# Optimization experiments

Hardware: AMD Instinct MI355X
Metric: run time of the kernel (lower is better)

The kernel has to match this reference:

```python
import jax, jax.numpy as jnp
import numpy as np

B, T, TC = 128, 300, 20          # batch, words per sentence, chars per word
DW, DC = 16, 32                  # word / char embedding dims
UC, UM = 32, 64                  # char-LSTM units, main-LSTM units
POS, PAR = 20, 8                 # extra feature dims
VW, VC = 1834, 132               # vocab sizes
DIN = DW + UC + POS + PAR        # 76, input dim of main BiLSTM


def setup_inputs() -> dict:
    key = jax.random.key(0)
    ks = jax.random.split(key, 16)
    s = 0.05
    f32 = jnp.float32
    return dict(
        word_in=jax.random.randint(ks[0], (B, T), 0, VW, dtype=jnp.int32),
        char_in=jax.random.randint(ks[1], (B, T, TC), 0, VC, dtype=jnp.int32),
        input_pos=jax.random.normal(ks[2], (B, T, POS), f32),
        input_par=jax.random.normal(ks[3], (B, T, PAR), f32),
        emb_wor=jax.random.normal(ks[4], (VW, DW), f32) * s,
        emb_char=jax.random.normal(ks[5], (VC, DC), f32) * s,
        char_Wx=jax.random.normal(ks[6], (DC, 4 * UC), f32) * s,
        char_Wh=jax.random.normal(ks[7], (UC, 4 * UC), f32) * s,
        char_b=jnp.zeros((4 * UC,), f32),
        fwd_Wx=jax.random.normal(ks[8], (DIN, 4 * UM), f32) * s,
        fwd_Wh=jax.random.normal(ks[9], (UM, 4 * UM), f32) * s,
        fwd_b=jnp.zeros((4 * UM,), f32),
        bwd_Wx=jax.random.normal(ks[10], (DIN, 4 * UM), f32) * s,
        bwd_Wh=jax.random.normal(ks[11], (UM, 4 * UM), f32) * s,
        bwd_b=jnp.zeros((4 * UM,), f32),
        dense_W=jax.random.normal(ks[12], (2 * UM, 4), f32) * s,
        dense_b=jnp.zeros((4,), f32),
    )


def _lstm(x, mask, Wx, Wh, b):
    """Masked Keras-style LSTM (gate order i,f,g,o). x:(N,S,D) mask:(N,S) bool.
    Masked steps carry state (Keras mask_zero semantics). Returns (N,S,U)."""
    U = Wh.shape[0]
    xz = jnp.einsum('nsd,df->nsf', x, Wx) + b  # hoist input projection out of scan

    def step(carry, inp):
        h, c = carry
        z_x, m = inp
        z = z_x + h @ Wh
        i, f, g, o = jnp.split(z, 4, axis=-1)
        c_new = jax.nn.sigmoid(f) * c + jax.nn.sigmoid(i) * jnp.tanh(g)
        h_new = jax.nn.sigmoid(o) * jnp.tanh(c_new)
        m = m[:, None]
        h = jnp.where(m, h_new, h)
        c = jnp.where(m, c_new, c)
        return (h, c), h

    N = x.shape[0]
    h0 = jnp.zeros((N, U), x.dtype)
    (_, _), hs = jax.lax.scan(step, (h0, h0),
                              (jnp.swapaxes(xz, 0, 1), jnp.swapaxes(mask, 0, 1)))
    return jnp.swapaxes(hs, 0, 1)


def reference(word_in, char_in, input_pos, input_par,
              emb_wor, emb_char, char_Wx, char_Wh, char_b,
              fwd_Wx, fwd_Wh, fwd_b, bwd_Wx, bwd_Wh, bwd_b,
              dense_W, dense_b):
    # word embeddings: (B,T,DW)
    ew = emb_wor[word_in]
    # char embeddings, TimeDistributed over words: (B*T, TC, DC)
    ec = emb_char[char_in].reshape(B * T, TC, DC)
    cmask = (char_in != 0).reshape(B * T, TC)
    # char LSTM, return_sequences=False -> final (last-valid) state
    ch = _lstm(ec, cmask, char_Wx, char_Wh, char_b)[:, -1, :].reshape(B, T, UC)
    # concat word emb, char encoding, extra features -> (B,T,DIN)
    x = jnp.concatenate([ew, ch, input_pos, input_par], axis=-1)
    wmask = word_in != 0
    hf = _lstm(x, wmask, fwd_Wx, fwd_Wh, fwd_b)
    hb = _lstm(x[:, ::-1], wmask[:, ::-1], bwd_Wx, bwd_Wh, bwd_b)[:, ::-1]
    h = jnp.concatenate([hf, hb], axis=-1)  # (B,T,2*UM)
    return jax.nn.softmax(h @ dense_W + dense_b, axis=-1)  # (B,T,4)
```

## Files before the change

### kernel.cpp

```cpp
#include <hip/hip_runtime.h>
#include <hip/hip_bf16.h>

#define B_ 128
#define T_ 300
#define TC_ 20
#define DW_ 16
#define DC_ 32
#define UC_ 32
#define UM_ 64
#define POS_ 20
#define PAR_ 8
#define VW_ 1834
#define VC_ 132
#define DIN_ 76
#define XS_ 80
#define NROW (B_*T_)

typedef _Float16 half_t;
typedef half_t h2 __attribute__((ext_vector_type(2)));

__device__ __forceinline__ float fast_sig(float x){
  return __builtin_amdgcn_rcpf(1.f + __expf(-x));
}
__device__ __forceinline__ float fast_tanh(float x){
  return __builtin_amdgcn_rcpf(1.f + __expf(-2.f*x))*2.f - 1.f;
}
__device__ __forceinline__ float dot2u(unsigned int a, unsigned int b, float acc){
  union{unsigned int u; h2 h;} x, y; x.u = a; y.u = b;
#if __has_builtin(__builtin_amdgcn_fdot2)
  return __builtin_amdgcn_fdot2(x.h, y.h, acc, false);
#else
  return acc + (float)x.h.x*(float)y.h.x + (float)x.h.y*(float)y.h.y;
#endif
}
__device__ __forceinline__ h2 u2h(unsigned int x){
  union{unsigned int u; h2 h;} t; t.u = x; return t.h;
}
__device__ __forceinline__ float us2f(unsigned short s){
  union{unsigned short s; half_t h;} x; x.s = s; return (float)x.h;
}
__device__ __forceinline__ unsigned int packh2(float a, float b){
  union{h2 h; unsigned int u;} cv; cv.h = h2{(half_t)a,(half_t)b}; return cv.u;
}

__global__ void k_prep(const float* __restrict__ emb_char, const float* __restrict__ char_Wx,
                       const float* __restrict__ char_b,  const float* __restrict__ char_Wh,
                       const float* __restrict__ Whf, const float* __restrict__ Whb,
                       const float* __restrict__ Wxf, const float* __restrict__ Wxb,
                       float* __restrict__ xzc, half_t* __restrict__ chT,
                       half_t* __restrict__ whT_h, half_t* __restrict__ wxT_h){
  int id = blockIdx.x*256 + threadIdx.x;
  if (id < 16896){
    int v = id >> 7, j = id & 127;
    float acc = char_b[j];
    #pragma unroll
    for (int k=0;k<DC_;k++) acc += emb_char[v*DC_+k]*char_Wx[k*(4*UC_)+j];
    xzc[id] = acc;
  } else if (id < 20992){
    int t = id - 16896;
    int j = t >> 5, k = t & 31;
    chT[t] = (half_t)char_Wh[k*(4*UC_)+j];
  } else if (id < 53760){
    int t = id - 20992;
    int dirr = t >> 14, j = (t >> 6) & 255, k = t & 63;
    const float* W = dirr ? Whb : Whf;
    whT_h[t] = (half_t)W[k*(4*UM_)+j];
  } else {
    int t = id - 53760;
    int dirr = t / 24576;
    int r = t % 24576;
    int jj = r / 96, k = r % 96;
    const float* W = dirr ? Wxb : Wxf;
    wxT_h[t] = (k < DIN_) ? (half_t)W[k*(4*UM_)+jj] : (half_t)0.f;
  }
}

__global__ __launch_bounds__(512,2) void k_char(const int* __restrict__ char_in,
        const float* __restrict__ xzc, const half_t* __restrict__ chT,
        const int* __restrict__ word_in, const float* __restrict__ emb_wor,
        const float* __restrict__ pos, const float* __restrict__ par,
        float* __restrict__ x){
  __shared__ unsigned int hbuf2[8][16];
  __shared__ float2 zex[8][64];
  __shared__ int sidx[8*TC_];
  const int tid = threadIdx.x;
  const int w8 = tid >> 6;
  const int lane = tid & 63;
  const int u = lane & 31;
  const int half = lane >> 5;
  const int seq = blockIdx.x*8 + w8;

  if (tid < 384){
    int r8 = tid / 48, c48 = tid % 48;
    int row = blockIdx.x*8 + r8;
    int col = (c48 < 16) ? c48 : (c48 + 32);
    float v;
    if (col < DW_)              v = emb_wor[word_in[row]*DW_ + col];
    else if (col < DW_+UC_+POS_) v = pos[row*POS_ + (col-(DW_+UC_))];
    else                         v = par[row*PAR_ + (col-(DW_+UC_+POS_))];
    x[row*XS_ + col] = v;
  }

  if (tid < 8*TC_) sidx[tid] = char_in[blockIdx.x*(8*TC_) + tid];
  if (half==0 && u<16) hbuf2[w8][u] = 0;

  unsigned int wa[16], wb[16];
  {
    const uint4* pa = reinterpret_cast<const uint4*>(chT + (half*64+u)*32);
    const uint4* pb = reinterpret_cast<const uint4*>(chT + (half*64+32+u)*32);
    #pragma unroll
    for (int q=0;q<4;q++){
      uint4 va = pa[q], vb = pb[q];
      wa[q*4+0]=va.x; wa[q*4+1]=va.y; wa[q*4+2]=va.z; wa[q*4+3]=va.w;
      wb[q*4+0]=vb.x; wb[q*4+1]=vb.y; wb[q*4+2]=vb.z; wb[q*4+3]=vb.w;
    }
  }
  __syncthreads();

  float h = 0.f, c = 0.f;
  int idx = sidx[w8*TC_ + 0];
  float za0 = xzc[idx*(4*UC_) + half*64 + u];
  float zb0 = xzc[idx*(4*UC_) + half*64 + 32 + u];

  for (int t=0; t<TC_; t++){
    int idxn = (t+1 < TC_) ? sidx[w8*TC_ + t+1] : 0;
    float zan = xzc[idxn*(4*UC_) + half*64 + u];
    float zbn = xzc[idxn*(4*UC_) + half*64 + 32 + u];

    float za = za0, zb = zb0;
    const uint4* hb = reinterpret_cast<const uint4*>(&hbuf2[w8][0]);
    uint4 q0=hb[0], q1=hb[1], q2=hb[2], q3=hb[3];
    unsigned int hu[16] = {q0.x,q0.y,q0.z,q0.w, q1.x,q1.y,q1.z,q1.w,
                           q2.x,q2.y,q2.z,q2.w, q3.x,q3.y,q3.z,q3.w};
    #pragma unroll
    for (int k=0;k<16;k++){
      za = dot2u(wa[k], hu[k], za);
      zb = dot2u(wb[k], hu[k], zb);
    }
    zex[w8][lane] = make_float2(za, zb);
    if (half == 0){
      float2 p = zex[w8][32+u];
      float zi = za, zf = zb, zg = p.x, zo = p.y;
      float cn = fast_sig(zf)*c + fast_sig(zi)*fast_tanh(zg);
      float hn = fast_sig(zo)*fast_tanh(cn);
      bool m = (idx != 0);
      c = m ? cn : c;
      h = m ? hn : h;
      reinterpret_cast<half_t*>(&hbuf2[w8][0])[u] = (half_t)h;
    }
    idx = idxn; za0 = zan; zb0 = zbn;
  }
  if (half == 0) x[seq*XS_ + DW_ + u] = h;
}

__global__ __launch_bounds__(512,2) void k_xz(const float* __restrict__ x,
      const half_t* __restrict__ wxT_h,
      const float* __restrict__ b_f, const float* __restrict__ b_b,
      half_t* __restrict__ xz){
  __shared__ unsigned int xs[16][40];
  const int j = threadIdx.x;
  const int jj = j & 255;
  const bool bwd = (j >= 256);
  const float bj = bwd ? b_b[jj] : b_f[jj];
  const int u = jj & 63, g = jj >> 6;
  const int ocol = (bwd ? 256 : 0) + u*4 + g;

  unsigned int wq[40];
  {
    const uint4* p = reinterpret_cast<const uint4*>(wxT_h + (size_t)((bwd?256:0)+jj)*96);
    #pragma unroll
    for (int q=0;q<10;q++){
      uint4 v = p[q];
      wq[q*4+0]=v.x; wq[q*4+1]=v.y; wq[q*4+2]=v.z; wq[q*4+3]=v.w;
    }
  }

  const int rowbase = blockIdx.x*16;
  for (int i=j; i<16*40; i+=512){
    int r = i/40, q = i%40;
    unsigned int pk = 0;
    if (q < 38){
      float v0 = x[(size_t)(rowbase+r)*XS_ + 2*q];
      float v1 = x[(size_t)(rowbase+r)*XS_ + 2*q+1];
      pk = packh2(v0, v1);
    }
    xs[r][q] = pk;
  }
  __syncthreads();

  for (int r=0; r<16; r++){
    const uint4* xr = reinterpret_cast<const uint4*>(&xs[r][0]);
    float acc = bj;
    #pragma unroll
    for (int q=0;q<10;q++){
      uint4 v = xr[q];
      acc = dot2u(wq[q*4+0], v.x, acc);
      acc = dot2u(wq[q*4+1], v.y, acc);
      acc = dot2u(wq[q*4+2], v.z, acc);
      acc = dot2u(wq[q*4+3], v.w, acc);
    }
    xz[(size_t)(rowbase+r)*512 + ocol] = (half_t)acc;
  }
}

__global__ __launch_bounds__(64,1) void k_rnn(const half_t* __restrict__ xz,
      const int* __restrict__ word_in, const half_t* __restrict__ whT_h,
      half_t* __restrict__ hcat){
  __shared__ half_t hbuf[64];
  __shared__ int wm[T_];
  const int l = threadIdx.x;
  const int dir = blockIdx.x & 1;
  const int b = blockIdx.x >> 1;

  unsigned int wt[4][32];
  #pragma unroll
  for (int g=0; g<4; g++){
    const uint4* p = reinterpret_cast<const uint4*>(whT_h + ((size_t)dir*256 + g*64 + l)*64);
    #pragma unroll
    for (int q=0;q<8;q++){
      uint4 v = p[q];
      wt[g][q*4+0]=v.x; wt[g][q*4+1]=v.y; wt[g][q*4+2]=v.z; wt[g][q*4+3]=v.w;
    }
  }
  for (int t=l; t<T_; t+=64) wm[t] = word_in[b*T_ + (dir ? (T_-1-t) : t)];
  hbuf[l] = (half_t)0.f;
  __syncthreads();

  float h = 0.f, c_ = 0.f;
  int row0 = b*T_ + (dir ? T_-1 : 0);
  const half_t* xp = xz + (size_t)row0*512 + dir*256 + l*4;
  const ptrdiff_t dstep = dir ? -512 : 512;
  half_t* hout = hcat + (size_t)row0*(2*UM_) + dir*UM_ + l;
  const ptrdiff_t hstep = dir ? -(2*UM_) : (2*UM_);

  ushort4 z0 = *reinterpret_cast<const ushort4*>(xp);
  ushort4 z1 = *reinterpret_cast<const ushort4*>(xp + dstep);
  half_t hh[10];
  const h2 zero2 = {(half_t)0.f, (half_t)0.f};

  for (int outer=0; outer<30; ++outer){
    #pragma unroll
    for (int s=0; s<10; ++s){
      const int t = outer*10 + s;
      ushort4 z2 = {0,0,0,0};
      if (t+2 < T_) z2 = *reinterpret_cast<const ushort4*>(xp + 2*dstep);

      const uint4* hb = reinterpret_cast<const uint4*>(hbuf);
      h2 aI0=zero2, aI1=zero2, aF0=zero2, aF1=zero2;
      h2 aG0=zero2, aG1=zero2, aO0=zero2, aO1=zero2;
      #pragma unroll
      for (int q=0;q<8;q++){
        uint4 hv = hb[q];
        h2 h0=u2h(hv.x), h1=u2h(hv.y), hx=u2h(hv.z), h3=u2h(hv.w);
        aI0 = u2h(wt[0][q*4+0])*h0 + aI0; aI1 = u2h(wt[0][q*4+1])*h1 + aI1;
        aI0 = u2h(wt[0][q*4+2])*hx + aI0; aI1 = u2h(wt[0][q*4+3])*h3 + aI1;
        aF0 = u2h(wt[1][q*4+0])*h0 + aF0; aF1 = u2h(wt[1][q*4+1])*h1 + aF1;
        aF0 = u2h(wt[1][q*4+2])*hx + aF0; aF1 = u2h(wt[1][q*4+3])*h3 + aF1;
        aG0 = u2h(wt[2][q*4+0])*h0 + aG0; aG1 = u2h(wt[2][q*4+1])*h1 + aG1;
        aG0 = u2h(wt[2][q*4+2])*hx + aG0; aG1 = u2h(wt[2][q*4+3])*h3 + aG1;
        aO0 = u2h(wt[3][q*4+0])*h0 + aO0; aO1 = u2h(wt[3][q*4+1])*h1 + aO1;
        aO0 = u2h(wt[3][q*4+2])*hx + aO0; aO1 = u2h(wt[3][q*4+3])*h3 + aO1;
      }
      float zi = us2f(z0.x) + (((float)aI0.x + (float)aI0.y) + ((float)aI1.x + (float)aI1.y));
      float zf = us2f(z0.y) + (((float)aF0.x + (float)aF0.y) + ((float)aF1.x + (float)aF1.y));
      float zg = us2f(z0.z) + (((float)aG0.x + (float)aG0.y) + ((float)aG1.x + (float)aG1.y));
      float zo = us2f(z0.w) + (((float)aO0.x + (float)aO0.y) + ((float)aO1.x + (float)aO1.y));

      int mw = wm[t];
      float cn = fast_sig(zf)*c_ + fast_sig(zi)*fast_tanh(zg);
      float hn = fast_sig(zo)*fast_tanh(cn);
      if (mw != 0){ c_ = cn; h = hn; }
      half_t hq = (half_t)h;
      hbuf[l] = hq;
      hh[s] = hq;
      z0 = z1; z1 = z2; xp += dstep;
    }
    #pragma unroll
    for (int s=0; s<10; ++s) hout[(ptrdiff_t)s * hstep] = hh[s];
    hout += (ptrdiff_t)10 * hstep;
  }
}

__global__ void k_dense(const half_t* __restrict__ hcat, const float* __restrict__ W,
                        const float* __restrict__ bias, float* __restrict__ out){
  int r = blockIdx.x*256 + threadIdx.x;
  const uint4* h4 = reinterpret_cast<const uint4*>(hcat + (size_t)r*(2*UM_));
  float a0=bias[0], a1=bias[1], a2=bias[2], a3=bias[3];
  #pragma unroll
  for (int k8=0;k8<16;k8++){
    uint4 v = h4[k8];
    unsigned int uu[4] = {v.x, v.y, v.z, v.w};
    #pragma unroll
    for (int e=0;e<4;e++){
      int k = k8*8 + e*2;
      float hA = us2f((unsigned short)(uu[e] & 0xffffu));
      float hB = us2f((unsigned short)(uu[e] >> 16));
      a0 += hA*W[k*4+0] + hB*W[(k+1)*4+0];
      a1 += hA*W[k*4+1] + hB*W[(k+1)*4+1];
      a2 += hA*W[k*4+2] + hB*W[(k+1)*4+2];
      a3 += hA*W[k*4+3] + hB*W[(k+1)*4+3];
    }
  }
  float mx = fmaxf(fmaxf(a0,a1), fmaxf(a2,a3));
  float e0=__expf(a0-mx), e1=__expf(a1-mx), e2=__expf(a2-mx), e3=__expf(a3-mx);
  float s = __builtin_amdgcn_rcpf(e0+e1+e2+e3);
  out[r*4+0]=e0*s; out[r*4+1]=e1*s; out[r*4+2]=e2*s; out[r*4+3]=e3*s;
}

extern "C" void kernel_launch(void* const* d_in, const int* in_sizes, int n_in,
                              void* d_out, int out_size, void* d_ws, size_t ws_size,
                              hipStream_t stream) {
  const int*   word_in  = (const int*)  d_in[0];
  const int*   char_in  = (const int*)  d_in[1];
  const float* inp_pos  = (const float*)d_in[2];
  const float* inp_par  = (const float*)d_in[3];
  const float* emb_wor  = (const float*)d_in[4];
  const float* emb_char = (const float*)d_in[5];
  const float* char_Wx  = (const float*)d_in[6];
  const float* char_Wh  = (const float*)d_in[7];
  const float* char_b   = (const float*)d_in[8];
  const float* fwd_Wx   = (const float*)d_in[9];
  const float* fwd_Wh   = (const float*)d_in[10];
  const float* fwd_b    = (const float*)d_in[11];
  const float* bwd_Wx   = (const float*)d_in[12];
  const float* bwd_Wh   = (const float*)d_in[13];
  const float* bwd_b    = (const float*)d_in[14];
  const float* dense_W  = (const float*)d_in[15];
  const float* dense_b  = (const float*)d_in[16];
  float* out = (float*)d_out;

  char* base = (char*)d_ws;
  float*  xw    = (float*)base;            base += (size_t)NROW*XS_*4;
  half_t* hcat  = (half_t*)base;           base += (size_t)NROW*128*2;
  float*  xzc   = (float*)base;            base += (size_t)VC_*128*4;
  half_t* chT   = (half_t*)base;           base += 128*32*2;
  half_t* whT_h = (half_t*)base;           base += 2*256*64*2;
  half_t* wxT_h = (half_t*)base;           base += 2*256*96*2;
  half_t* xzw   = (half_t*)base;

  k_prep <<<402, 256, 0, stream>>>(emb_char, char_Wx, char_b, char_Wh,
                                   fwd_Wh, bwd_Wh, fwd_Wx, bwd_Wx,
                                   xzc, chT, whT_h, wxT_h);
  k_char <<<NROW/8, 512, 0, stream>>>(char_in, xzc, chT,
                                      word_in, emb_wor, inp_pos, inp_par, xw);
  k_xz   <<<NROW/16, 512, 0, stream>>>(xw, wxT_h, fwd_b, bwd_b, xzw);
  k_rnn  <<<2*B_, 64, 0, stream>>>(xzw, word_in, whT_h, hcat);
  k_dense<<<NROW/256, 256, 0, stream>>>(hcat, dense_W, dense_b, out);
}
```

Baseline: 313.0 us.

## Process four sequences per RNN wavefront to amortize weight registers and latency

```diff
diff --git a/kernel.cpp b/kernel.cpp
--- a/kernel.cpp
+++ b/kernel.cpp
@@ -32,9 +32,6 @@
 #else
   return acc + (float)x.h.x*(float)y.h.x + (float)x.h.y*(float)y.h.y;
 #endif
-}
-__device__ __forceinline__ h2 u2h(unsigned int x){
-  union{unsigned int u; h2 h;} t; t.u = x; return t.h;
 }
 __device__ __forceinline__ float us2f(unsigned short s){
   union{unsigned short s; half_t h;} x; x.s = s; return (float)x.h;
@@ -206,11 +203,11 @@
 __global__ __launch_bounds__(64,1) void k_rnn(const half_t* __restrict__ xz,
       const int* __restrict__ word_in, const half_t* __restrict__ whT_h,
       half_t* __restrict__ hcat){
-  __shared__ half_t hbuf[64];
-  __shared__ int wm[T_];
+  __shared__ half_t hbuf[4][64];
+  __shared__ int wm[4][T_];
   const int l = threadIdx.x;
   const int dir = blockIdx.x & 1;
-  const int b = blockIdx.x >> 1;
+  const int bg = blockIdx.x >> 1;
 
   unsigned int wt[4][32];
   #pragma unroll
@@ -222,62 +219,94 @@
       wt[g][q*4+0]=v.x; wt[g][q*4+1]=v.y; wt[g][q*4+2]=v.z; wt[g][q*4+3]=v.w;
     }
   }
-  for (int t=l; t<T_; t+=64) wm[t] = word_in[b*T_ + (dir ? (T_-1-t) : t)];
-  hbuf[l] = (half_t)0.f;
+  const ptrdiff_t dstep = dir ? -512 : 512;
+  const ptrdiff_t hstep = dir ? -(2*UM_) : (2*UM_);
+  const half_t* xp[4];
+  half_t* hout[4];
+  #pragma unroll
+  for (int c=0;c<4;c++){
+    int b = bg*4 + c;
+    for (int t=l; t<T_; t+=64) wm[c][t] = word_in[b*T_ + (dir ? (T_-1-t) : t)];
+    hbuf[c][l] = (half_t)0.f;
+    int row0 = b*T_ + (dir ? T_-1 : 0);
+    xp[c]   = xz   + (size_t)row0*512 + dir*256 + l*4;
+    hout[c] = hcat + (size_t)row0*(2*UM_) + dir*UM_ + l;
+  }
   __syncthreads();
 
-  float h = 0.f, c_ = 0.f;
-  int row0 = b*T_ + (dir ? T_-1 : 0);
-  const half_t* xp = xz + (size_t)row0*512 + dir*256 + l*4;
-  const ptrdiff_t dstep = dir ? -512 : 512;
-  half_t* hout = hcat + (size_t)row0*(2*UM_) + dir*UM_ + l;
-  const ptrdiff_t hstep = dir ? -(2*UM_) : (2*UM_);
-
-  ushort4 z0 = *reinterpret_cast<const ushort4*>(xp);
-  ushort4 z1 = *reinterpret_cast<const ushort4*>(xp + dstep);
-  half_t hh[10];
-  const h2 zero2 = {(half_t)0.f, (half_t)0.f};
+  float h[4]  = {0.f,0.f,0.f,0.f};
+  float cc[4] = {0.f,0.f,0.f,0.f};
+  ushort4 z0[4], z1[4];
+  #pragma unroll
+  for (int c=0;c<4;c++){
+    z0[c] = *reinterpret_cast<const ushort4*>(xp[c]);
+    z1[c] = *reinterpret_cast<const ushort4*>(xp[c] + dstep);
+  }
+  half_t hh[4][10];
 
   for (int outer=0; outer<30; ++outer){
     #pragma unroll
     for (int s=0; s<10; ++s){
       const int t = outer*10 + s;
-      ushort4 z2 = {0,0,0,0};
-      if (t+2 < T_) z2 = *reinterpret_cast<const ushort4*>(xp + 2*dstep);
-
-      const uint4* hb = reinterpret_cast<const uint4*>(hbuf);
-      h2 aI0=zero2, aI1=zero2, aF0=zero2, aF1=zero2;
-      h2 aG0=zero2, aG1=zero2, aO0=zero2, aO1=zero2;
+      ushort4 z2[4];
+      #pragma unroll
+      for (int c=0;c<4;c++){
+        z2[c] = ushort4{0,0,0,0};
+        if (t+2 < T_) z2[c] = *reinterpret_cast<const ushort4*>(xp[c] + 2*dstep);
+      }
+
+      float aI0[4],aI1[4],aF0[4],aF1[4],aG0[4],aG1[4],aO0[4],aO1[4];
+      #pragma unroll
+      for (int c=0;c<4;c++){ aI0[c]=0.f;aI1[c]=0.f;aF0[c]=0.f;aF1[c]=0.f;
+                             aG0[c]=0.f;aG1[c]=0.f;aO0[c]=0.f;aO1[c]=0.f; }
       #pragma unroll
       for (int q=0;q<8;q++){
-        uint4 hv = hb[q];
-        h2 h0=u2h(hv.x), h1=u2h(hv.y), hx=u2h(hv.z), h3=u2h(hv.w);
-        aI0 = u2h(wt[0][q*4+0])*h0 + aI0; aI1 = u2h(wt[0][q*4+1])*h1 + aI1;
-        aI0 = u2h(wt[0][q*4+2])*hx + aI0; aI1 = u2h(wt[0][q*4+3])*h3 + aI1;
-        aF0 = u2h(wt[1][q*4+0])*h0 + aF0; aF1 = u2h(wt[1][q*4+1])*h1 + aF1;
-        aF0 = u2h(wt[1][q*4+2])*hx + aF0; aF1 = u2h(wt[1][q*4+3])*h3 + aF1;
-        aG0 = u2h(wt[2][q*4+0])*h0 + aG0; aG1 = u2h(wt[2][q*4+1])*h1 + aG1;
-        aG0 = u2h(wt[2][q*4+2])*hx + aG0; aG1 = u2h(wt[2][q*4+3])*h3 + aG1;
-        aO0 = u2h(wt[3][q*4+0])*h0 + aO0; aO1 = u2h(wt[3][q*4+1])*h1 + aO1;
-        aO0 = u2h(wt[3][q*4+2])*hx + aO0; aO1 = u2h(wt[3][q*4+3])*h3 + aO1;
+        uint4 hv[4];
+        #pragma unroll
+        for (int c=0;c<4;c++)
+          hv[c] = reinterpret_cast<const uint4*>(&hbuf[c][0])[q];
+        #pragma unroll
+        for (int c=0;c<4;c++){
+          aI0[c] = dot2u(wt[0][q*4+0], hv[c].x, aI0[c]);
+          aI1[c] = dot2u(wt[0][q*4+1], hv[c].y, aI1[c]);
+          aI0[c] = dot2u(wt[0][q*4+2], hv[c].z, aI0[c]);
+          aI1[c] = dot2u(wt[0][q*4+3], hv[c].w, aI1[c]);
+          aF0[c] = dot2u(wt[1][q*4+0], hv[c].x, aF0[c]);
+          aF1[c] = dot2u(wt[1][q*4+1], hv[c].y, aF1[c]);
+          aF0[c] = dot2u(wt[1][q*4+2], hv[c].z, aF0[c]);
+          aF1[c] = dot2u(wt[1][q*4+3], hv[c].w, aF1[c]);
+          aG0[c] = dot2u(wt[2][q*4+0], hv[c].x, aG0[c]);
+          aG1[c] = dot2u(wt[2][q*4+1], hv[c].y, aG1[c]);
+          aG0[c] = dot2u(wt[2][q*4+2], hv[c].z, aG0[c]);
+          aG1[c] = dot2u(wt[2][q*4+3], hv[c].w, aG1[c]);
+          aO0[c] = dot2u(wt[3][q*4+0], hv[c].x, aO0[c]);
+          aO1[c] = dot2u(wt[3][q*4+1], hv[c].y, aO1[c]);
+          aO0[c] = dot2u(wt[3][q*4+2], hv[c].z, aO0[c]);
+          aO1[c] = dot2u(wt[3][q*4+3], hv[c].w, aO1[c]);
+        }
       }
-      float zi = us2f(z0.x) + (((float)aI0.x + (float)aI0.y) + ((float)aI1.x + (float)aI1.y));
-      float zf = us2f(z0.y) + (((float)aF0.x + (float)aF0.y) + ((float)aF1.x + (float)aF1.y));
-      float zg = us2f(z0.z) + (((float)aG0.x + (float)aG0.y) + ((float)aG1.x + (float)aG1.y));
-      float zo = us2f(z0.w) + (((float)aO0.x + (float)aO0.y) + ((float)aO1.x + (float)aO1.y));
-
-      int mw = wm[t];
-      float cn = fast_sig(zf)*c_ + fast_sig(zi)*fast_tanh(zg);
-      float hn = fast_sig(zo)*fast_tanh(cn);
-      if (mw != 0){ c_ = cn; h = hn; }
-      half_t hq = (half_t)h;
-      hbuf[l] = hq;
-      hh[s] = hq;
-      z0 = z1; z1 = z2; xp += dstep;
-    }
-    #pragma unroll
-    for (int s=0; s<10; ++s) hout[(ptrdiff_t)s * hstep] = hh[s];
-    hout += (ptrdiff_t)10 * hstep;
+      #pragma unroll
+      for (int c=0;c<4;c++){
+        float zi = us2f(z0[c].x) + (aI0[c]+aI1[c]);
+        float zf = us2f(z0[c].y) + (aF0[c]+aF1[c]);
+        float zg = us2f(z0[c].z) + (aG0[c]+aG1[c]);
+        float zo = us2f(z0[c].w) + (aO0[c]+aO1[c]);
+        int mw = wm[c][t];
+        float cn = fast_sig(zf)*cc[c] + fast_sig(zi)*fast_tanh(zg);
+        float hn = fast_sig(zo)*fast_tanh(cn);
+        if (mw != 0){ cc[c] = cn; h[c] = hn; }
+        half_t hq = (half_t)h[c];
+        hbuf[c][l] = hq;
+        hh[c][s] = hq;
+        z0[c] = z1[c]; z1[c] = z2[c]; xp[c] += dstep;
+      }
+    }
+    #pragma unroll
+    for (int c=0;c<4;c++){
+      #pragma unroll
+      for (int s=0; s<10; ++s) hout[c][(ptrdiff_t)s * hstep] = hh[c][s];
+      hout[c] += (ptrdiff_t)10 * hstep;
+    }
   }
 }
 
@@ -344,6 +373,6 @@
   k_char <<<NROW/8, 512, 0, stream>>>(char_in, xzc, chT,
                                       word_in, emb_wor, inp_pos, inp_par, xw);
   k_xz   <<<NROW/16, 512, 0, stream>>>(xw, wxT_h, fwd_b, bwd_b, xzw);
-  k_rnn  <<<2*B_, 64, 0, stream>>>(xzw, word_in, whT_h, hcat);
+  k_rnn  <<<64, 64, 0, stream>>>(xzw, word_in, whT_h, hcat);
   k_dense<<<NROW/256, 256, 0, stream>>>(hcat, dense_W, dense_b, out);
 }
```

New measurement: 685.3 us. 119% more time.
